# Kernel tuning notes

Measured on AMD Instinct MI355X. Metric: run time of the kernel, lower is better.

## Reference

```python
import jax, jax.numpy as jnp
import numpy as np
from jax import lax


def conv3x3(x, w):
    # x: (B,C,H,W), w: (O,I,3,3); stride 1, padding 1, no bias
    return lax.conv_general_dilated(x, w, (1, 1), 'SAME',
                                    dimension_numbers=('NCHW', 'OIHW', 'NCHW'))


def group_norm(x, w, b, groups=32, eps=1e-5):
    B, C, H, W = x.shape
    xg = x.reshape(B, groups, C // groups, H, W)
    mu = xg.mean(axis=(2, 3, 4), keepdims=True)
    var = xg.var(axis=(2, 3, 4), keepdims=True)
    xg = (xg - mu) * lax.rsqrt(var + eps)
    return xg.reshape(B, C, H, W) * w[None, :, None, None] + b[None, :, None, None]


def to_patches(x, p1, p2):
    # 'b c (h p1) (w p2) -> (b h w) c (p1 p2)'
    B, C, H, W = x.shape
    h, w = H // p1, W // p2
    x = x.reshape(B, C, h, p1, w, p2).transpose(0, 2, 4, 1, 3, 5)
    return x.reshape(B * h * w, C, p1 * p2)


def from_patches(x, B, h, w, p1, p2):
    # '(b h w) c (p1 p2) -> b c (h p1) (w p2)'
    C = x.shape[1]
    x = x.reshape(B, h, w, C, p1, p2).transpose(0, 3, 1, 4, 2, 5)
    return x.reshape(B, C, h * p1, w * p2)


def setup_inputs() -> dict:
    key = jax.random.key(0)
    ks = jax.random.split(key, 5)
    B, C, H, W = 8, 256, 128, 128
    inter = 256
    s = 0.05  # keep conv outputs in a sane range
    return {
        'x_low': jax.random.normal(ks[0], (B, C, H, W), jnp.float32),
        'x_high': jax.random.normal(ks[1], (B, C, H, W), jnp.float32),
        'w_q': jax.random.normal(ks[2], (inter, C, 3, 3), jnp.float32) * s,
        'gq_w': jnp.ones((inter,), jnp.float32),
        'gq_b': jnp.zeros((inter,), jnp.float32),
        'w_k': jax.random.normal(ks[3], (inter, C, 3, 3), jnp.float32) * s,
        'gk_w': jnp.ones((inter,), jnp.float32),
        'gk_b': jnp.zeros((inter,), jnp.float32),
        'w_o': jax.random.normal(ks[4], (C, inter, 3, 3), jnp.float32) * s,
        'go_w': jnp.ones((C,), jnp.float32),
        'go_b': jnp.zeros((C,), jnp.float32),
        'p1': 8,
        'p2': 8,
    }


def reference(x_low, x_high, w_q, gq_w, gq_b, w_k, gk_w, gk_b, w_o, go_w, go_b, p1, p2):
    B, C, H, W = x_low.shape
    inter = w_q.shape[0]
    h, w = H // p1, W // p2
    # q, k: (B*h*w, inter, T) with T = p1*p2
    q = to_patches(group_norm(conv3x3(x_low, w_q), gq_w, gq_b), p1, p2)
    k = to_patches(group_norm(conv3x3(x_high, w_k), gk_w, gk_b), p1, p2)
    q = q.transpose(0, 2, 1)                                  # (N, T, inter)
    attn = jnp.matmul(q, k) / jnp.sqrt(jnp.float32(inter))    # (N, T, T)
    attn = jax.nn.softmax(attn, axis=-1)
    out = jnp.matmul(attn, k.transpose(0, 2, 1))              # (N, T, inter)
    out = from_patches(out.transpose(0, 2, 1), B, h, w, p1, p2)
    return group_norm(conv3x3(out + x_low, w_o), go_w, go_b)
```

## Files before the change

kernel.cpp:

```cpp
#include <hip/hip_runtime.h>

using u16 = unsigned short;
using u32 = unsigned int;

typedef short bfrag8 __attribute__((ext_vector_type(8)));
typedef float f32x4  __attribute__((ext_vector_type(4)));

__device__ __forceinline__ void unpack8(const int4 v, float f[8]) {
  u32 a = (u32)v.x, b = (u32)v.y, c = (u32)v.z, d = (u32)v.w;
  f[0] = __uint_as_float(a << 16);
  f[1] = __uint_as_float(a & 0xffff0000u);
  f[2] = __uint_as_float(b << 16);
  f[3] = __uint_as_float(b & 0xffff0000u);
  f[4] = __uint_as_float(c << 16);
  f[5] = __uint_as_float(c & 0xffff0000u);
  f[6] = __uint_as_float(d << 16);
  f[7] = __uint_as_float(d & 0xffff0000u);
}

__device__ __forceinline__ u16 f2bf(float f) {
  u32 u = __float_as_uint(f);
  u32 r = u + 0x7fffu + ((u >> 16) & 1u);
  return (u16)(r >> 16);
}

__device__ __forceinline__ void gload_lds16(const void* g, void* l) {
  __builtin_amdgcn_global_load_lds(
      (const __attribute__((address_space(1))) void*)g,
      (__attribute__((address_space(3))) void*)l, 16, 0, 0);
}

__global__ __launch_bounds__(256) void wprep(
    const float* __restrict__ wq, const float* __restrict__ wk, const float* __restrict__ wo,
    u16* __restrict__ dq, u16* __restrict__ dk, u16* __restrict__ dwo)
{
  const float* s = (blockIdx.y == 0) ? wq : (blockIdx.y == 1) ? wk : wo;
  u16* d = (blockIdx.y == 0) ? dq : (blockIdx.y == 1) ? dk : dwo;
  int id = blockIdx.x * 256 + threadIdx.x;
  int e = id * 4;
  int tap = e >> 16;
  int rem = e & 65535;
  int oc = rem >> 8, ic = rem & 255;
  u16 o[4];
#pragma unroll
  for (int j = 0; j < 4; ++j)
    o[j] = f2bf(s[((size_t)oc * 256 + ic + j) * 9 + tap]);
  *reinterpret_cast<uint2*>(d + e) = *reinterpret_cast<uint2*>(o);
}

__global__ __launch_bounds__(256) void xpose(
    const float* __restrict__ xa, const float* __restrict__ xb,
    u16* __restrict__ oa, u16* __restrict__ ob)
{
  const int row = blockIdx.x, b = blockIdx.y;
  const float* src = blockIdx.z ? xb : xa;
  u16* dst = blockIdx.z ? ob : oa;
  const int t = threadIdx.x;
  const int px4 = (t >> 3) * 4;
  const int c8 = (t & 7) * 8;
#pragma unroll
  for (int p = 0; p < 4; ++p) {
    int c0 = p * 64 + c8;
    float4 v[8];
#pragma unroll
    for (int j = 0; j < 8; ++j)
      v[j] = *reinterpret_cast<const float4*>(src + ((size_t)b * 256 + c0 + j) * 16384 + row * 128 + px4);
#pragma unroll
    for (int e = 0; e < 4; ++e) {
      u16 o[8];
      o[0] = f2bf(e==0?v[0].x:e==1?v[0].y:e==2?v[0].z:v[0].w);
      o[1] = f2bf(e==0?v[1].x:e==1?v[1].y:e==2?v[1].z:v[1].w);
      o[2] = f2bf(e==0?v[2].x:e==1?v[2].y:e==2?v[2].z:v[2].w);
      o[3] = f2bf(e==0?v[3].x:e==1?v[3].y:e==2?v[3].z:v[3].w);
      o[4] = f2bf(e==0?v[4].x:e==1?v[4].y:e==2?v[4].z:v[4].w);
      o[5] = f2bf(e==0?v[5].x:e==1?v[5].y:e==2?v[5].z:v[5].w);
      o[6] = f2bf(e==0?v[6].x:e==1?v[6].y:e==2?v[6].z:v[6].w);
      o[7] = f2bf(e==0?v[7].x:e==1?v[7].y:e==2?v[7].z:v[7].w);
      *reinterpret_cast<int4*>(dst + (((size_t)b * 128 + row) * 128 + px4 + e) * 256 + c0) =
          *reinterpret_cast<int4*>(o);
    }
  }
}

__global__ __launch_bounds__(256, 3) void conv_mfma(
    const u16* __restrict__ X, const u16* __restrict__ W2, u16* __restrict__ Y,
    float* __restrict__ part, u16* __restrict__ kTout)
{
  __shared__ __attribute__((aligned(16))) char csm[49920];

  const int t = threadIdx.x;
  const int l = t & 63;
  const int wv = t >> 6;
  const int id = blockIdx.x;
  const int u = (id & 7) * 256 + (id >> 3);
  const int bb = u >> 8;
  const int y0 = (u >> 1) & 127;
  const int ocblk = u & 1;
  const int oc0 = ocblk * 128;
  const int och = wv >> 1, pxh = wv & 1;
  const int lc = l & 15, lq = l >> 4;
  const int sa = (lc >> 1) & 3;

  f32x4 acc[4][4];
#pragma unroll
  for (int m = 0; m < 4; ++m)
#pragma unroll
    for (int n = 0; n < 4; ++n) acc[m][n] = (f32x4){0.f, 0.f, 0.f, 0.f};

  const size_t xplane = (size_t)bb * (128 * 128 * 256);

  {
    int4 z = {0, 0, 0, 0};
    if (t < 24) {
      int q = t & 3, sel = (t >> 2) & 1, kh = t >> 3;
      int cidx = sel ? 129 : 0;
      *reinterpret_cast<int4*>(csm + ((kh * 132 + cidx) * 4 + q) * 16) = z;
    }
    if (y0 == 0)
      for (int s = t; s < 528; s += 256) *reinterpret_cast<int4*>(csm + s * 16) = z;
    if (y0 == 127)
      for (int s = t; s < 528; s += 256) *reinterpret_cast<int4*>(csm + 16896 + s * 16) = z;
  }

  auto stageA = [&](int tap, int buf, int ic0) {
#pragma unroll
    for (int i = 0; i < 2; ++i) {
      int idx = t + i * 256;
      int oc = idx >> 2, q = idx & 3;
      int qs = q ^ ((oc >> 1) & 3);
      const u16* src = W2 + (((size_t)(tap * 256 + oc0 + oc)) << 8) + ic0 + qs * 8;
      gload_lds16(src, csm + 25344 + buf * 8192 + (i * 256 + (t & ~63)) * 16);
    }
  };
  auto stageB = [&](int ic0) {
#pragma unroll
    for (int i = 0; i < 6; ++i) {
      int idx = t + i * 256;
      int kh = idx >> 9;
      int row = y0 - 1 + kh;
      if (row >= 0 && row < 128) {
        int px = (idx & 511) >> 2, q = idx & 3;
        int qs = q ^ (((px + 1) >> 1) & 3);
        const u16* src = X + xplane + (((size_t)(row * 128 + px)) << 8) + ic0 + qs * 8;
        gload_lds16(src, csm + 64 + kh * 256 + (i * 256 + (t & ~63)) * 16);
      }
    }
  };

  bfrag8 af0[4], xf0[4], af1[4], xf1[4];

#define READF(TAP, AF, XF)                                                    \
  {                                                                           \
    const int kh_ = (TAP) / 3, kw_ = (TAP) % 3, buf_ = (TAP) % 3;             \
    const int sb_ = ((lc + kw_) >> 1) & 3;                                    \
    _Pragma("unroll")                                                         \
    for (int m = 0; m < 4; ++m)                                               \
      AF[m] = *reinterpret_cast<const bfrag8*>(csm + 25344 + buf_ * 8192 +    \
                  ((och * 64 + m * 16 + lc) * 4 + (lq ^ sa)) * 16);           \
    _Pragma("unroll")                                                         \
    for (int n = 0; n < 4; ++n) {                                             \
      int S_ = pxh * 64 + n * 16 + lc + kw_;                                  \
      XF[n] = *reinterpret_cast<const bfrag8*>(csm + kh_ * 8448 + S_ * 64 +   \
                  (lq ^ sb_) * 16);                                           \
    }                                                                         \
  }

#define DOMFMA(AF, XF)                                                        \
  {                                                                           \
    _Pragma("unroll")                                                         \
    for (int m = 0; m < 4; ++m)                                               \
      _Pragma("unroll")                                                       \
      for (int n = 0; n < 4; ++n)                                             \
        acc[m][n] = __builtin_amdgcn_mfma_f32_16x16x32_bf16(AF[m], XF[n],     \
                                                            acc[m][n], 0, 0, 0); \
  }

  stageB(0);
  stageA(0, 0, 0);
  stageA(1, 1, 0);
  __syncthreads();

  for (int chunk = 0; chunk < 8; ++chunk) {
    const int ic0 = chunk * 32;
    READF(0, af0, xf0);
#pragma unroll
    for (int tap = 0; tap < 9; ++tap) {
      asm volatile("s_waitcnt lgkmcnt(0)" ::: "memory");
      __builtin_amdgcn_sched_barrier(0);
      if (tap <= 6) stageA(tap + 2, (tap + 2) % 3, ic0);
      if (tap <= 6) {
        asm volatile("s_waitcnt vmcnt(2)" ::: "memory");
      } else if (tap == 7) {
        asm volatile("s_waitcnt vmcnt(0)" ::: "memory");
      }
      __builtin_amdgcn_sched_barrier(0);
      __builtin_amdgcn_s_barrier();
      __builtin_amdgcn_sched_barrier(0);

      if (tap < 8) {
        if (tap & 1) { READF(tap + 1, af0, xf0); }
        else         { READF(tap + 1, af1, xf1); }
      }
      __builtin_amdgcn_s_setprio(1);
      if (tap & 1) { DOMFMA(af1, xf1); }
      else         { DOMFMA(af0, xf0); }
      __builtin_amdgcn_s_setprio(0);
    }
    if (chunk < 7) {
      stageA(0, 0, ic0 + 32);
      stageA(1, 1, ic0 + 32);
      stageB(ic0 + 32);
      __syncthreads();
    }
  }
#undef READF
#undef DOMFMA

  u16* Ost = (u16*)csm;
  float* sst = (float*)(csm + 34816);
  const int chb = och * 64 + lq * 4;
  const int pxb = pxh * 64 + lc;
  __syncthreads();
#pragma unroll
  for (int m = 0; m < 4; ++m)
#pragma unroll
    for (int n = 0; n < 4; ++n) {
      u32 lo = (u32)f2bf(acc[m][n][0]) | ((u32)f2bf(acc[m][n][1]) << 16);
      u32 hi = (u32)f2bf(acc[m][n][2]) | ((u32)f2bf(acc[m][n][3]) << 16);
      uint2 pk = {lo, hi};
      *reinterpret_cast<uint2*>(&Ost[(pxb + n * 16) * 136 + chb + m * 16]) = pk;
    }
#pragma unroll
  for (int m = 0; m < 4; ++m)
#pragma unroll
    for (int r = 0; r < 4; ++r) {
      float s  = acc[m][0][r] + acc[m][1][r] + acc[m][2][r] + acc[m][3][r];
      float ss = acc[m][0][r] * acc[m][0][r] + acc[m][1][r] * acc[m][1][r] +
                 acc[m][2][r] * acc[m][2][r] + acc[m][3][r] * acc[m][3][r];
#pragma unroll
      for (int off = 1; off < 16; off <<= 1) {
        s  += __shfl_xor(s, off);
        ss += __shfl_xor(ss, off);
      }
      if (lc == 0) {
        int c = och * 64 + m * 16 + lq * 4 + r;
        sst[pxh * 256 + c]       = s;
        sst[pxh * 256 + 128 + c] = ss;
      }
    }
  __syncthreads();

  if (t < 128) {
    float s  = sst[t]       + sst[256 + t];
    float ss = sst[128 + t] + sst[384 + t];
    size_t pb = (((size_t)bb * 128 + y0) * 256 + oc0 + t) * 2;
    part[pb]     = s;
    part[pb + 1] = ss;
  }
#pragma unroll
  for (int s8 = 0; s8 < 8; ++s8) {
    int pix = s8 * 16 + (t >> 4);
    int sub = t & 15;
    int4 v = *reinterpret_cast<const int4*>(&Ost[pix * 136 + sub * 8]);
    *reinterpret_cast<int4*>(Y + xplane + (((size_t)(y0 * 128 + pix)) << 8) + oc0 + sub * 8) = v;
  }

  if (kTout) {
    const size_t outbase = ((size_t)(bb * 16 + (y0 >> 3)) * 8 + (y0 & 7)) * 32768;
    const int half = t >> 7;
    const int cl = t & 127;
#pragma unroll
    for (int i = 0; i < 8; ++i) {
      int pw = i * 2 + half;
      u16 o[8];
#pragma unroll
      for (int j = 0; j < 8; ++j) o[j] = Ost[(pw * 8 + j) * 136 + cl];
      *reinterpret_cast<int4*>(kTout + outbase + (size_t)(pw * 256 + oc0 + cl) * 8) =
          *reinterpret_cast<int4*>(o);
    }
  }
}

__global__ __launch_bounds__(256) void gnstat2c(
    const float* __restrict__ part0, float* __restrict__ stat0,
    const float* __restrict__ part1, float* __restrict__ stat1)
{
  const float* part = (blockIdx.z == 0) ? part0 : part1;
  float* stat = (blockIdx.z == 0) ? stat0 : stat1;
  const int g = blockIdx.x, b = blockIdx.y;
  const int t = threadIdx.x;
  const int row = t >> 1, half = t & 1;
  const float* p = part + (((size_t)b * 128 + row) * 256 + g * 8 + half * 4) * 2;
  float4 v0 = *reinterpret_cast<const float4*>(p);
  float4 v1 = *reinterpret_cast<const float4*>(p + 4);
  float s  = v0.x + v0.z + v1.x + v1.z;
  float ss = v0.y + v0.w + v1.y + v1.w;
#pragma unroll
  for (int off = 1; off < 64; off <<= 1) {
    s  += __shfl_xor(s, off);
    ss += __shfl_xor(ss, off);
  }
  __shared__ float Ls[4], Lss[4];
  if ((t & 63) == 0) { Ls[t >> 6] = s; Lss[t >> 6] = ss; }
  __syncthreads();
  if (t == 0) {
    float S  = Ls[0] + Ls[1] + Ls[2] + Ls[3];
    float SS = Lss[0] + Lss[1] + Lss[2] + Lss[3];
    float mean = S * (1.f / 131072.f);
    float var  = SS * (1.f / 131072.f) - mean * mean;
    stat[b * 32 + g]       = mean;
    stat[256 + b * 32 + g] = rsqrtf(var + 1e-5f);
  }
}

#define OST 272
__global__ __launch_bounds__(256, 3) void attn_mfma(
    const u16* __restrict__ yq, const u16* __restrict__ yk,
    const u16* __restrict__ kT, const u16* __restrict__ xl,
    const float* __restrict__ statq, const float* __restrict__ statk,
    const float* __restrict__ gqw, const float* __restrict__ gqb,
    const float* __restrict__ gkw, const float* __restrict__ gkb,
    u16* __restrict__ resid)
{
  __shared__ __attribute__((aligned(16))) u16 smem[64 * OST + 4 * 16 * 72];
  u16* Ost = smem;
  u16* Pls = smem + 64 * OST;

  const int n = blockIdx.x;
  const int b = n >> 8, ph = (n >> 4) & 15, pw = n & 15;
  const int t = threadIdx.x, l = t & 63, w = t >> 6;
  const int lc = l & 15, lg = l >> 4;

  auto tokaddr = [&](int tok) -> size_t {
    return (((size_t)(b * 128 + ph * 8 + (tok >> 3))) * 128 + pw * 8 + (tok & 7)) * 256;
  };

  const size_t qa = tokaddr(16 * w + lc) + lg * 8;
  bfrag8 aF[8];
#pragma unroll
  for (int ks = 0; ks < 8; ++ks) {
    int c0 = lg * 8 + ks * 32;
    int g = ks * 4 + lg;
    float meanq = statq[b * 32 + g], rstdq = statq[256 + b * 32 + g];
    float rstdk = statk[256 + b * 32 + g];
    int4 v = *reinterpret_cast<const int4*>(yq + qa + ks * 32);
    float f[8]; unpack8(v, f);
    float4 w0 = *reinterpret_cast<const float4*>(gqw + c0);
    float4 w1 = *reinterpret_cast<const float4*>(gqw + c0 + 4);
    float4 b0 = *reinterpret_cast<const float4*>(gqb + c0);
    float4 b1 = *reinterpret_cast<const float4*>(gqb + c0 + 4);
    float4 k0 = *reinterpret_cast<const float4*>(gkw + c0);
    float4 k1 = *reinterpret_cast<const float4*>(gkw + c0 + 4);
    float ww[8] = {w0.x, w0.y, w0.z, w0.w, w1.x, w1.y, w1.z, w1.w};
    float bb[8] = {b0.x, b0.y, b0.z, b0.w, b1.x, b1.y, b1.z, b1.w};
    float kk[8] = {k0.x, k0.y, k0.z, k0.w, k1.x, k1.y, k1.z, k1.w};
    u16 o[8];
#pragma unroll
    for (int j = 0; j < 8; ++j) {
      float Aq = rstdq * ww[j];
      float Bq = bb[j] - meanq * Aq;
      float Ak = rstdk * kk[j];
      o[j] = f2bf((f[j] * Aq + Bq) * Ak);
    }
    aF[ks] = *reinterpret_cast<bfrag8*>(o);
  }

  f32x4 sacc[4];
#pragma unroll
  for (int nt = 0; nt < 4; ++nt) sacc[nt] = (f32x4){0.f, 0.f, 0.f, 0.f};

#pragma unroll
  for (int nt = 0; nt < 4; ++nt) {
    const size_t ka = tokaddr(nt * 16 + lc) + lg * 8;
    bfrag8 bF[8];
#pragma unroll
    for (int ks = 0; ks < 8; ++ks)
      bF[ks] = *reinterpret_cast<const bfrag8*>(yk + ka + ks * 32);
#pragma unroll
    for (int ks = 0; ks < 8; ++ks)
      sacc[nt] = __builtin_amdgcn_mfma_f32_16x16x32_bf16(aF[ks], bF[ks], sacc[nt], 0, 0, 0);
  }

  u16* Pw = Pls + w * (16 * 72);
#pragma unroll
  for (int r = 0; r < 4; ++r) {
    float m0 = fmaxf(fmaxf(sacc[0][r], sacc[1][r]), fmaxf(sacc[2][r], sacc[3][r]));
    m0 = fmaxf(m0, __shfl_xor(m0, 1));
    m0 = fmaxf(m0, __shfl_xor(m0, 2));
    m0 = fmaxf(m0, __shfl_xor(m0, 4));
    m0 = fmaxf(m0, __shfl_xor(m0, 8));
    float p0 = __expf((sacc[0][r] - m0) * 0.0625f);
    float p1 = __expf((sacc[1][r] - m0) * 0.0625f);
    float p2 = __expf((sacc[2][r] - m0) * 0.0625f);
    float p3 = __expf((sacc[3][r] - m0) * 0.0625f);
    float s0 = p0 + p1 + p2 + p3;
    s0 += __shfl_xor(s0, 1);
    s0 += __shfl_xor(s0, 2);
    s0 += __shfl_xor(s0, 4);
    s0 += __shfl_xor(s0, 8);
    float inv = 1.f / s0;
    int prow = (lg * 4 + r) * 72;
    Pw[prow + 0 * 16 + lc] = f2bf(p0 * inv);
    Pw[prow + 1 * 16 + lc] = f2bf(p1 * inv);
    Pw[prow + 2 * 16 + lc] = f2bf(p2 * inv);
    Pw[prow + 3 * 16 + lc] = f2bf(p3 * inv);
  }

  bfrag8 pA[2];
#pragma unroll
  for (int js = 0; js < 2; ++js)
    pA[js] = *reinterpret_cast<const bfrag8*>(Pw + lc * 72 + js * 32 + lg * 8);

  f32x4 pacc[16];
#pragma unroll
  for (int ct = 0; ct < 16; ++ct) pacc[ct] = (f32x4){0.f, 0.f, 0.f, 0.f};

#pragma unroll
  for (int ct = 0; ct < 16; ++ct) {
    bfrag8 vB[2];
#pragma unroll
    for (int js = 0; js < 2; ++js)
      vB[js] = *reinterpret_cast<const bfrag8*>(
          kT + ((size_t)((b * 16 + ph) * 8 + js * 4 + lg)) * 32768 +
          (size_t)(pw * 256 + ct * 16 + lc) * 8);
#pragma unroll
    for (int js = 0; js < 2; ++js)
      pacc[ct] = __builtin_amdgcn_mfma_f32_16x16x32_bf16(pA[js], vB[js], pacc[ct], 0, 0, 0);
  }

#pragma unroll
  for (int ct = 0; ct < 16; ++ct) {
    int c = ct * 16 + lc;
    int g = c >> 3;
    float mean = statk[b * 32 + g], rstd = statk[256 + b * 32 + g];
    float A = rstd * gkw[c];
    float Bv = gkb[c] - mean * A;
#pragma unroll
    for (int r = 0; r < 4; ++r)
      Ost[(16 * w + lg * 4 + r) * OST + ct * 16 + lc] = f2bf(fmaf(pacc[ct][r], A, Bv));
  }
  __syncthreads();

#pragma unroll
  for (int s = 0; s < 8; ++s) {
    int px_ = t >> 5;
    int c16 = t & 31;
    size_t g = (((size_t)b * 128 + ph * 8 + s) * 128 + pw * 8 + px_) * 256 + c16 * 8;
    int4 o = *reinterpret_cast<const int4*>(&Ost[(s * 8 + px_) * OST + c16 * 8]);
    int4 r = *reinterpret_cast<const int4*>(xl + g);
    float fo[8], fr[8]; unpack8(o, fo); unpack8(r, fr);
    u16 pk[8];
#pragma unroll
    for (int j = 0; j < 8; ++j) pk[j] = f2bf(fo[j] + fr[j]);
    *reinterpret_cast<int4*>(resid + g) = *reinterpret_cast<int4*>(pk);
  }
}

__global__ __launch_bounds__(256) void gnapply_t(
    const u16* __restrict__ Y, const float* __restrict__ stat,
    const float* __restrict__ gw, const float* __restrict__ gb,
    float* __restrict__ out)
{
  const int row = blockIdx.x, b = blockIdx.y;
  const int t = threadIdx.x;
  const int px4 = (t & 31) * 4;
  const int c8 = (t >> 5) * 8;
#pragma unroll
  for (int p = 0; p < 4; ++p) {
    int c0 = p * 64 + c8;
    int g = c0 >> 3;
    float mean = stat[b * 32 + g], rstd = stat[256 + b * 32 + g];
    float A[8], Bv[8];
#pragma unroll
    for (int j = 0; j < 8; ++j) {
      A[j] = rstd * gw[c0 + j];
      Bv[j] = gb[c0 + j] - mean * A[j];
    }
    float vals[4][8];
#pragma unroll
    for (int e = 0; e < 4; ++e) {
      int4 v = *reinterpret_cast<const int4*>(Y + (((size_t)b * 128 + row) * 128 + px4 + e) * 256 + c0);
      float f[8]; unpack8(v, f);
#pragma unroll
      for (int j = 0; j < 8; ++j) vals[e][j] = fmaf(f[j], A[j], Bv[j]);
    }
#pragma unroll
    for (int j = 0; j < 8; ++j) {
      float4 o = {vals[0][j], vals[1][j], vals[2][j], vals[3][j]};
      *reinterpret_cast<float4*>(out + ((size_t)b * 256 + c0 + j) * 16384 + row * 128 + px4) = o;
    }
  }
}

extern "C" void kernel_launch(void* const* d_in, const int* in_sizes, int n_in,
                              void* d_out, int out_size, void* d_ws, size_t ws_size,
                              hipStream_t stream)
{
  const float* x_low  = (const float*)d_in[0];
  const float* x_high = (const float*)d_in[1];
  const float* w_q    = (const float*)d_in[2];
  const float* gq_w   = (const float*)d_in[3];
  const float* gq_b   = (const float*)d_in[4];
  const float* w_k    = (const float*)d_in[5];
  const float* gk_w   = (const float*)d_in[6];
  const float* gk_b   = (const float*)d_in[7];
  const float* w_o    = (const float*)d_in[8];
  const float* go_w   = (const float*)d_in[9];
  const float* go_b   = (const float*)d_in[10];
  float* out = (float*)d_out;

  char* ws = (char*)d_ws;
  const size_t slot = 67108864;
  u16* xl  = (u16*)(ws + 0 * slot);
  u16* xh  = (u16*)(ws + 1 * slot);
  u16* yq  = (u16*)(ws + 2 * slot);
  u16* yk  = (u16*)(ws + 3 * slot);
  u16* kT  = (u16*)(ws + 4 * slot);
  u16* W2q = (u16*)(ws + 5 * slot);
  u16* W2k = W2q + 589824;
  u16* W2o = W2k + 589824;
  float* partq = (float*)(ws + 5 * slot + 3 * 1179648);
  float* partk = partq + 524288;
  float* parto = partk + 524288;
  float* statq = parto + 524288;
  float* statk = statq + 512;
  float* stato = statk + 512;

  wprep<<<dim3(576, 3), 256, 0, stream>>>(w_q, w_k, w_o, W2q, W2k, W2o);
  xpose<<<dim3(128, 8, 2), 256, 0, stream>>>(x_low, x_high, xl, xh);
  conv_mfma<<<2048, 256, 0, stream>>>(xl, W2q, yq, partq, nullptr);
  conv_mfma<<<2048, 256, 0, stream>>>(xh, W2k, yk, partk, kT);
  gnstat2c<<<dim3(32, 8, 2), 256, 0, stream>>>(partq, statq, partk, statk);
  attn_mfma<<<2048, 256, 0, stream>>>(yq, yk, kT, xl, statq, statk,
                                      gq_w, gq_b, gk_w, gk_b, xh);
  conv_mfma<<<2048, 256, 0, stream>>>(xh, W2o, xl, parto, nullptr);
  gnstat2c<<<dim3(32, 8, 1), 256, 0, stream>>>(parto, stato, parto, stato);
  gnapply_t<<<dim3(128, 8), 256, 0, stream>>>(xl, stato, go_w, go_b, out);
}
```

Before: 669.1 us.

## Shrink conv LDS footprint and fragment registers to raise occupancy to four blocks

Removes the padded halo columns from the staged input rows by clamping column indices and zeroing edge fragments in registers, and cuts the weight buffer ring from three slots to two. This lowers shared memory per block and drops the double-buffered fragment registers, so launch bounds can request four blocks per CU instead of three. In exchange the pipeline gets shallower: weight staging now has only one tap of lead time, each tap waits for all outstanding loads before the barrier, and fragment reads are no longer overlapped with the previous tap's MFMAs.

```diff
diff --git a/kernel.cpp b/kernel.cpp
--- a/kernel.cpp
+++ b/kernel.cpp
@@ -82,11 +82,11 @@
   }
 }
 
-__global__ __launch_bounds__(256, 3) void conv_mfma(
+__global__ __launch_bounds__(256, 4) void conv_mfma(
     const u16* __restrict__ X, const u16* __restrict__ W2, u16* __restrict__ Y,
     float* __restrict__ part, u16* __restrict__ kTout)
 {
-  __shared__ __attribute__((aligned(16))) char csm[49920];
+  __shared__ __attribute__((aligned(16))) char csm[40960];
 
   const int t = threadIdx.x;
   const int l = t & 63;
@@ -111,15 +111,10 @@
 
   {
     int4 z = {0, 0, 0, 0};
-    if (t < 24) {
-      int q = t & 3, sel = (t >> 2) & 1, kh = t >> 3;
-      int cidx = sel ? 129 : 0;
-      *reinterpret_cast<int4*>(csm + ((kh * 132 + cidx) * 4 + q) * 16) = z;
-    }
     if (y0 == 0)
-      for (int s = t; s < 528; s += 256) *reinterpret_cast<int4*>(csm + s * 16) = z;
+      for (int s = t; s < 512; s += 256) reinterpret_cast<int4*>(csm)[s] = z;
     if (y0 == 127)
-      for (int s = t; s < 528; s += 256) *reinterpret_cast<int4*>(csm + 16896 + s * 16) = z;
+      for (int s = t; s < 512; s += 256) reinterpret_cast<int4*>(csm + 16384)[s] = z;
   }
 
   auto stageA = [&](int tap, int buf, int ic0) {
@@ -129,7 +124,7 @@
       int oc = idx >> 2, q = idx & 3;
       int qs = q ^ ((oc >> 1) & 3);
       const u16* src = W2 + (((size_t)(tap * 256 + oc0 + oc)) << 8) + ic0 + qs * 8;
-      gload_lds16(src, csm + 25344 + buf * 8192 + (i * 256 + (t & ~63)) * 16);
+      gload_lds16(src, csm + 24576 + buf * 8192 + (i * 256 + (t & ~63)) * 16);
     }
   };
   auto stageB = [&](int ic0) {
@@ -139,39 +134,49 @@
       int kh = idx >> 9;
       int row = y0 - 1 + kh;
       if (row >= 0 && row < 128) {
-        int px = (idx & 511) >> 2, q = idx & 3;
-        int qs = q ^ (((px + 1) >> 1) & 3);
+        int inner = idx & 511;
+        int px = inner >> 2, q = inner & 3;
+        int qs = q ^ ((px >> 1) & 3);
         const u16* src = X + xplane + (((size_t)(row * 128 + px)) << 8) + ic0 + qs * 8;
-        gload_lds16(src, csm + 64 + kh * 256 + (i * 256 + (t & ~63)) * 16);
+        gload_lds16(src, csm + kh * 8192 + ((i * 256 + (t & ~63)) & 511) * 16);
       }
     }
   };
 
-  bfrag8 af0[4], xf0[4], af1[4], xf1[4];
-
-#define READF(TAP, AF, XF)                                                    \
+  bfrag8 af[4], xf[4];
+
+#define READF(TAP)                                                            \
   {                                                                           \
-    const int kh_ = (TAP) / 3, kw_ = (TAP) % 3, buf_ = (TAP) % 3;             \
-    const int sb_ = ((lc + kw_) >> 1) & 3;                                    \
+    const int kh_ = (TAP) / 3, kw_ = (TAP) % 3, abuf_ = (TAP) & 1;            \
     _Pragma("unroll")                                                         \
     for (int m = 0; m < 4; ++m)                                               \
-      AF[m] = *reinterpret_cast<const bfrag8*>(csm + 25344 + buf_ * 8192 +    \
+      af[m] = *reinterpret_cast<const bfrag8*>(csm + 24576 + abuf_ * 8192 +   \
                   ((och * 64 + m * 16 + lc) * 4 + (lq ^ sa)) * 16);           \
     _Pragma("unroll")                                                         \
     for (int n = 0; n < 4; ++n) {                                             \
       int S_ = pxh * 64 + n * 16 + lc + kw_;                                  \
-      XF[n] = *reinterpret_cast<const bfrag8*>(csm + kh_ * 8448 + S_ * 64 +   \
-                  (lq ^ sb_) * 16);                                           \
+      int col = S_ - 1;                                                       \
+      col = col < 0 ? 0 : (col > 127 ? 127 : col);                            \
+      xf[n] = *reinterpret_cast<const bfrag8*>(csm + kh_ * 8192 + col * 64 +  \
+                  (lq ^ ((col >> 1) & 3)) * 16);                              \
     }                                                                         \
   }
 
-#define DOMFMA(AF, XF)                                                        \
+#define FIXX(TAP)                                                             \
+  {                                                                           \
+    const int kw_ = (TAP) % 3;                                                \
+    bfrag8 bz = {};                                                           \
+    if (kw_ == 0) { if (pxh == 0 && lc == 0)  xf[0] = bz; }                   \
+    if (kw_ == 2) { if (pxh == 1 && lc == 15) xf[3] = bz; }                   \
+  }
+
+#define DOMFMA()                                                              \
   {                                                                           \
     _Pragma("unroll")                                                         \
     for (int m = 0; m < 4; ++m)                                               \
       _Pragma("unroll")                                                       \
       for (int n = 0; n < 4; ++n)                                             \
-        acc[m][n] = __builtin_amdgcn_mfma_f32_16x16x32_bf16(AF[m], XF[n],     \
+        acc[m][n] = __builtin_amdgcn_mfma_f32_16x16x32_bf16(af[m], xf[n],     \
                                                             acc[m][n], 0, 0, 0); \
   }
 
@@ -182,29 +187,21 @@
 
   for (int chunk = 0; chunk < 8; ++chunk) {
     const int ic0 = chunk * 32;
-    READF(0, af0, xf0);
 #pragma unroll
     for (int tap = 0; tap < 9; ++tap) {
+      READF(tap);
       asm volatile("s_waitcnt lgkmcnt(0)" ::: "memory");
       __builtin_amdgcn_sched_barrier(0);
-      if (tap <= 6) stageA(tap + 2, (tap + 2) % 3, ic0);
-      if (tap <= 6) {
-        asm volatile("s_waitcnt vmcnt(2)" ::: "memory");
-      } else if (tap == 7) {
-        asm volatile("s_waitcnt vmcnt(0)" ::: "memory");
-      }
+      FIXX(tap);
+      if (tap >= 1 && tap <= 7) stageA(tap + 1, (tap + 1) & 1, ic0);
+      __builtin_amdgcn_s_setprio(1);
+      DOMFMA();
+      __builtin_amdgcn_s_setprio(0);
+      __builtin_amdgcn_sched_barrier(0);
+      asm volatile("s_waitcnt vmcnt(0)" ::: "memory");
       __builtin_amdgcn_sched_barrier(0);
       __builtin_amdgcn_s_barrier();
       __builtin_amdgcn_sched_barrier(0);
-
-      if (tap < 8) {
-        if (tap & 1) { READF(tap + 1, af0, xf0); }
-        else         { READF(tap + 1, af1, xf1); }
-      }
-      __builtin_amdgcn_s_setprio(1);
-      if (tap & 1) { DOMFMA(af1, xf1); }
-      else         { DOMFMA(af0, xf0); }
-      __builtin_amdgcn_s_setprio(0);
     }
     if (chunk < 7) {
       stageA(0, 0, ic0 + 32);
@@ -214,6 +211,7 @@
     }
   }
 #undef READF
+#undef FIXX
 #undef DOMFMA
 
   u16* Ost = (u16*)csm;
```

Result: slower. 699.9 us (+4.6%).
